# Kernel optimization log

Measured on AMD Instinct MI355X. Metric: run time of the kernel, lower is better.

Reference implementation:

```python
import jax, jax.numpy as jnp
import numpy as np

N, F_IN, F_OUT, HEADS = 8192, 128, 64, 2
NEG_INF = -1e10
LEAKY_ALPHA = 0.2


def setup_inputs() -> dict:
    key = jax.random.key(0)
    k_x, k_a, k_w, k_as, k_an = jax.random.split(key, 5)
    X = jax.random.normal(k_x, (N, F_IN), dtype=jnp.float32)
    A = (jax.random.uniform(k_a, (N, N)) < 0.004).astype(jnp.float32)
    A = jnp.maximum(A, jnp.eye(N, dtype=jnp.float32))
    kernels = jax.random.normal(k_w, (HEADS, F_IN, F_OUT), dtype=jnp.float32) * (1.0 / np.sqrt(F_IN))
    biases = jnp.zeros((HEADS, F_OUT), dtype=jnp.float32)
    attn_self = jax.random.normal(k_as, (HEADS, F_OUT), dtype=jnp.float32) * (1.0 / np.sqrt(F_OUT))
    attn_neigh = jax.random.normal(k_an, (HEADS, F_OUT), dtype=jnp.float32) * (1.0 / np.sqrt(F_OUT))
    return {"X": X, "A": A, "kernels": kernels, "biases": biases,
            "attn_self": attn_self, "attn_neigh": attn_neigh}


def reference(X, A, kernels, biases, attn_self, attn_neigh):
    # per-head linear projection: [H, N, F_OUT]
    feats = jnp.einsum('nf,hfo->hno', X, kernels)
    # additive attention logits (GAT): e_ij = leakyrelu(a_s^T h_i + a_n^T h_j)
    a_s = jnp.einsum('hno,ho->hn', feats, attn_self)    # [H, N]
    a_n = jnp.einsum('hno,ho->hn', feats, attn_neigh)   # [H, N]
    dense = a_s[:, :, None] + a_n[:, None, :]           # [H, N, N]
    dense = jnp.where(dense > 0, dense, LEAKY_ALPHA * dense)
    dense = dense + NEG_INF * (1.0 - A)                 # adjacency mask
    attn = jax.nn.softmax(dense, axis=-1)               # [H, N, N]
    # dropout_rate = 0.0 -> dropout is identity
    node_feats = jnp.einsum('hnm,hmo->hno', attn, feats) + biases[:, None, :]
    out = jnp.mean(node_feats, axis=0)                  # 'average' head reduction
    return jax.nn.relu(out)                             # activation='relu'
```

## Files before the change

### kernel.cpp

```cpp
#include <hip/hip_runtime.h>
#include <hip/hip_bf16.h>
#include <cfloat>

#define N_NODES 8192
#define F_IN    128
#define F_OUT   64
#define HEADS   2
#define LEAKY   0.2f
#define ROWS    8
#define CAP     128

typedef float f32x4 __attribute__((ext_vector_type(4)));

__global__ __launch_bounds__(128) void feats_kernel(
    const float* __restrict__ X, const float* __restrict__ W,
    const float* __restrict__ attn_self, const float* __restrict__ attn_neigh,
    float* __restrict__ feats, float* __restrict__ a_s, float* __restrict__ a_n)
{
    __shared__ float Xs[ROWS][F_IN];
    const int tid = threadIdx.x;
    const int n0  = blockIdx.x * ROWS;

    for (int k = tid; k < ROWS * F_IN; k += 128) {
        Xs[k / F_IN][k % F_IN] = X[(size_t)(n0 + k / F_IN) * F_IN + (k % F_IN)];
    }
    __syncthreads();

    const int h = tid >> 6;
    const int o = tid & 63;
    const float* Wh = W + (size_t)h * F_IN * F_OUT;

    float acc[ROWS];
    #pragma unroll
    for (int r = 0; r < ROWS; ++r) acc[r] = 0.f;

    for (int f = 0; f < F_IN; ++f) {
        float wv = Wh[f * F_OUT + o];
        #pragma unroll
        for (int r = 0; r < ROWS; ++r) acc[r] += Xs[r][f] * wv;
    }

    const float asv = attn_self[h * F_OUT + o];
    const float anv = attn_neigh[h * F_OUT + o];
    #pragma unroll
    for (int r = 0; r < ROWS; ++r) {
        const int n = n0 + r;
        const float v = acc[r];
        feats[((size_t)h * N_NODES + n) * F_OUT + o] = v;
        float s = v * asv;
        float t = v * anv;
        #pragma unroll
        for (int off = 32; off > 0; off >>= 1) {
            s += __shfl_down(s, off);
            t += __shfl_down(t, off);
        }
        if (o == 0) {
            a_s[h * N_NODES + n] = s;
            a_n[h * N_NODES + n] = t;
        }
    }
}

__global__ __launch_bounds__(256) void fused_row_kernel(
    const float* __restrict__ A, const float* __restrict__ feats,
    const float* __restrict__ a_s, const float* __restrict__ a_n,
    const float* __restrict__ biases, float* __restrict__ out)
{
    __shared__ int   jj_s[4][CAP];
    __shared__ float w0_s[4][CAP];
    __shared__ float w1_s[4][CAP];

    const int wave = threadIdx.x >> 6;
    const int lane = threadIdx.x & 63;
    const int row  = blockIdx.x * 4 + wave;

    int*   jj = jj_s[wave];
    float* w0 = w0_s[wave];
    float* w1 = w1_s[wave];

    const unsigned long long lt = (1ULL << lane) - 1ULL;

    const f32x4* Arow = (const f32x4*)(A + (size_t)row * N_NODES);
    int base = 0;
    f32x4 cur = __builtin_nontemporal_load(&Arow[lane]);
    for (int it = 0; it < 32; ++it) {
        f32x4 nxt = cur;
        if (it < 31) nxt = __builtin_nontemporal_load(&Arow[(it + 1) * 64 + lane]);
        const int col0 = (it * 64 + lane) * 4;
        #pragma unroll
        for (int comp = 0; comp < 4; ++comp) {
            const bool nz = cur[comp] > 0.5f;
            const unsigned long long m = __ballot(nz);
            if (nz) {
                const int p = base + __popcll(m & lt);
                if (p < CAP) jj[p] = col0 + comp;
            }
            base += __popcll(m);
        }
        cur = nxt;
    }
    const int count = min(base, CAP);

    const float as0 = a_s[row];
    const float as1 = a_s[N_NODES + row];
    float m0 = -FLT_MAX, m1 = -FLT_MAX;
    for (int k = lane; k < count; k += 64) {
        const int j = jj[k];
        float e0 = as0 + a_n[j];            e0 = e0 > 0.f ? e0 : LEAKY * e0;
        float e1 = as1 + a_n[N_NODES + j];  e1 = e1 > 0.f ? e1 : LEAKY * e1;
        w0[k] = e0; w1[k] = e1;
        m0 = fmaxf(m0, e0); m1 = fmaxf(m1, e1);
    }
    #pragma unroll
    for (int off = 32; off > 0; off >>= 1) {
        m0 = fmaxf(m0, __shfl_xor(m0, off));
        m1 = fmaxf(m1, __shfl_xor(m1, off));
    }
    float s0 = 0.f, s1 = 0.f;
    for (int k = lane; k < count; k += 64) {
        const float p0 = __expf(w0[k] - m0); w0[k] = p0; s0 += p0;
        const float p1 = __expf(w1[k] - m1); w1[k] = p1; s1 += p1;
    }
    #pragma unroll
    for (int off = 32; off > 0; off >>= 1) {
        s0 += __shfl_xor(s0, off);
        s1 += __shfl_xor(s1, off);
    }

    const float* f0 = feats;
    const float* f1 = feats + (size_t)N_NODES * F_OUT;
    float acc0 = 0.f, acc1 = 0.f;
    for (int k = 0; k < count; ++k) {
        const int   j  = jj[k];
        const float p0 = w0[k];
        const float p1 = w1[k];
        acc0 += p0 * f0[(size_t)j * F_OUT + lane];
        acc1 += p1 * f1[(size_t)j * F_OUT + lane];
    }
    const float v = 0.5f * ((acc0 / s0 + biases[lane]) +
                            (acc1 / s1 + biases[F_OUT + lane]));
    out[(size_t)row * F_OUT + lane] = v > 0.f ? v : 0.f;
}

extern "C" void kernel_launch(void* const* d_in, const int* in_sizes, int n_in,
                              void* d_out, int out_size, void* d_ws, size_t ws_size,
                              hipStream_t stream) {
    const float* X          = (const float*)d_in[0];
    const float* A          = (const float*)d_in[1];
    const float* W          = (const float*)d_in[2];
    const float* biases     = (const float*)d_in[3];
    const float* attn_self  = (const float*)d_in[4];
    const float* attn_neigh = (const float*)d_in[5];
    float* out = (float*)d_out;

    float* feats = (float*)d_ws;
    float* a_s   = feats + (size_t)HEADS * N_NODES * F_OUT;
    float* a_n   = a_s + HEADS * N_NODES;

    feats_kernel<<<N_NODES / ROWS, 128, 0, stream>>>(
        X, W, attn_self, attn_neigh, feats, a_s, a_n);
    fused_row_kernel<<<N_NODES / 4, 256, 0, stream>>>(
        A, feats, a_s, a_n, biases, out);
}
```

Baseline: 371.1 us.

## Interleave head feats layout, deepen adjacency prefetch, unroll neighbor gather by two

Stores feats and attention logits interleaved by head, so each neighbor's two head rows sit in one contiguous 512-byte span and a_n pairs load as one float2. The adjacency row scan now double-buffers four 16-byte loads per lane per stage, which keeps more reads in flight. The gather loop handles two neighbors per iteration to expose more memory parallelism. The cost is higher register use for the prefetch buffers. The kernel is dominated by streaming the 256 MB dense A matrix, so gains may be bounded by bandwidth.

Result: no change. 370.1 us (median of 2 runs) (-0.3%).

```diff
diff --git a/kernel.cpp b/kernel.cpp
--- a/kernel.cpp
+++ b/kernel.cpp
@@ -46,7 +46,7 @@
     for (int r = 0; r < ROWS; ++r) {
         const int n = n0 + r;
         const float v = acc[r];
-        feats[((size_t)h * N_NODES + n) * F_OUT + o] = v;
+        feats[((size_t)n * 2 + h) * F_OUT + o] = v;
         float s = v * asv;
         float t = v * anv;
         #pragma unroll
@@ -55,8 +55,8 @@
             t += __shfl_down(t, off);
         }
         if (o == 0) {
-            a_s[h * N_NODES + n] = s;
-            a_n[h * N_NODES + n] = t;
+            a_s[n * 2 + h] = s;
+            a_n[n * 2 + h] = t;
         }
     }
 }
@@ -81,33 +81,45 @@
     const unsigned long long lt = (1ULL << lane) - 1ULL;
 
     const f32x4* Arow = (const f32x4*)(A + (size_t)row * N_NODES);
+    f32x4 buf[2][4];
+    #pragma unroll
+    for (int q = 0; q < 4; ++q)
+        buf[0][q] = __builtin_nontemporal_load(&Arow[q * 64 + lane]);
+
     int base = 0;
-    f32x4 cur = __builtin_nontemporal_load(&Arow[lane]);
-    for (int it = 0; it < 32; ++it) {
-        f32x4 nxt = cur;
-        if (it < 31) nxt = __builtin_nontemporal_load(&Arow[(it + 1) * 64 + lane]);
-        const int col0 = (it * 64 + lane) * 4;
+    #pragma unroll
+    for (int g = 0; g < 8; ++g) {
+        const int cb = g & 1, nb = cb ^ 1;
+        if (g < 7) {
+            #pragma unroll
+            for (int q = 0; q < 4; ++q)
+                buf[nb][q] = __builtin_nontemporal_load(
+                    &Arow[(g + 1) * 256 + q * 64 + lane]);
+        }
         #pragma unroll
-        for (int comp = 0; comp < 4; ++comp) {
-            const bool nz = cur[comp] > 0.5f;
-            const unsigned long long m = __ballot(nz);
-            if (nz) {
-                const int p = base + __popcll(m & lt);
-                if (p < CAP) jj[p] = col0 + comp;
+        for (int q = 0; q < 4; ++q) {
+            const f32x4 v = buf[cb][q];
+            const int col0 = (g * 256 + q * 64 + lane) * 4;
+            #pragma unroll
+            for (int comp = 0; comp < 4; ++comp) {
+                const bool nz = v[comp] > 0.5f;
+                const unsigned long long m = __ballot(nz);
+                if (nz) {
+                    const int p = base + __popcll(m & lt);
+                    if (p < CAP) jj[p] = col0 + comp;
+                }
+                base += __popcll(m);
             }
-            base += __popcll(m);
         }
-        cur = nxt;
     }
     const int count = min(base, CAP);
 
-    const float as0 = a_s[row];
-    const float as1 = a_s[N_NODES + row];
+    const float2 as = ((const float2*)a_s)[row];
     float m0 = -FLT_MAX, m1 = -FLT_MAX;
     for (int k = lane; k < count; k += 64) {
-        const int j = jj[k];
-        float e0 = as0 + a_n[j];            e0 = e0 > 0.f ? e0 : LEAKY * e0;
-        float e1 = as1 + a_n[N_NODES + j];  e1 = e1 > 0.f ? e1 : LEAKY * e1;
+        const float2 an = ((const float2*)a_n)[jj[k]];
+        float e0 = as.x + an.x;  e0 = e0 > 0.f ? e0 : LEAKY * e0;
+        float e1 = as.y + an.y;  e1 = e1 > 0.f ? e1 : LEAKY * e1;
         w0[k] = e0; w1[k] = e1;
         m0 = fmaxf(m0, e0); m1 = fmaxf(m1, e1);
     }
@@ -127,15 +139,24 @@
         s1 += __shfl_xor(s1, off);
     }
 
-    const float* f0 = feats;
-    const float* f1 = feats + (size_t)N_NODES * F_OUT;
     float acc0 = 0.f, acc1 = 0.f;
-    for (int k = 0; k < count; ++k) {
-        const int   j  = jj[k];
-        const float p0 = w0[k];
-        const float p1 = w1[k];
-        acc0 += p0 * f0[(size_t)j * F_OUT + lane];
-        acc1 += p1 * f1[(size_t)j * F_OUT + lane];
+    int k = 0;
+    for (; k + 1 < count; k += 2) {
+        const int j0 = jj[k], j1 = jj[k + 1];
+        const float* r0 = feats + (size_t)j0 * 128;
+        const float* r1 = feats + (size_t)j1 * 128;
+        const float p00 = w0[k],     p10 = w1[k];
+        const float p01 = w0[k + 1], p11 = w1[k + 1];
+        const float f00 = r0[lane], f01 = r0[64 + lane];
+        const float f10 = r1[lane], f11 = r1[64 + lane];
+        acc0 += p00 * f00; acc1 += p10 * f01;
+        acc0 += p01 * f10; acc1 += p11 * f11;
+    }
+    if (k < count) {
+        const int j = jj[k];
+        const float* r = feats + (size_t)j * 128;
+        acc0 += w0[k] * r[lane];
+        acc1 += w1[k] * r[64 + lane];
     }
     const float v = 0.5f * ((acc0 / s0 + biases[lane]) +
                             (acc1 / s1 + biases[F_OUT + lane]));
```
